# Performance work log

Measured on AMD Instinct MI355X. Metric: run time of the kernel, lower is better.

## Reference

```python
import jax, jax.numpy as jnp
import numpy as np

WIN = 9
EPS = 1e-05


def _box_sum(x, win=WIN):
    # Separable 3D box-filter sum: mathematically identical to conv3d with a
    pad = win // 2
    for axis in range(3):  # spatial axes D, H, W
        kshape = [1, 1, 1]
        kshape[axis] = win
        filt = jnp.ones((1, 1, *kshape), dtype=x.dtype)  # OIDHW
        padding = [(pad, pad) if i == axis else (0, 0) for i in range(3)]
        x = jax.lax.conv_general_dilated(
            x, filt, window_strides=(1, 1, 1), padding=padding,
            dimension_numbers=('NCDHW', 'OIDHW', 'NCDHW'))
    return x


def setup_inputs() -> dict:
    key = jax.random.key(0)
    k1, k2 = jax.random.split(key)
    shape = (2, 1, 160, 192, 224)
    y_true = jax.random.uniform(k1, shape, dtype=jnp.float32)
    y_pred = jax.random.uniform(k2, shape, dtype=jnp.float32)
    return {"y_true": y_true, "y_pred": y_pred}


def reference(y_true, y_pred):
    ii, ji = y_true, y_pred
    win_size = jnp.asarray(float(WIN ** 3), dtype=ii.dtype)

    i_sum = _box_sum(ii)
    j_sum = _box_sum(ji)
    i2_sum = _box_sum(ii * ii)
    j2_sum = _box_sum(ji * ji)
    ij_sum = _box_sum(ii * ji)

    ui = i_sum / win_size
    uj = j_sum / win_size
    cross = ij_sum - uj * i_sum - ui * j_sum + ui * uj * win_size
    i_var = jnp.maximum(i2_sum - 2 * ui * i_sum + ui * ui * win_size, EPS)
    j_var = jnp.maximum(j2_sum - 2 * uj * j_sum + uj * uj * win_size, EPS)
    return -jnp.mean(cross * cross / (i_var * j_var))
```

## Files before the change

kernel.cpp:

```cpp
#include <hip/hip_runtime.h>

namespace {

constexpr int BD = 2;
constexpr int DD = 160, HH = 192, WW = 224;
constexpr float INV_WIN = 1.0f / 729.0f;
constexpr float EPSV = 1e-5f;

constexpr int TH = 16, TW = 16;
constexpr int DC = 16;
constexpr int NREAL = DC + 8;
constexpr int NPAIR = NREAL / 2;
constexpr int NCH = DD / DC;
constexpr int GX = WW / TW;
constexpr int GY = HH / TH;
constexpr int GZ = BD * NCH;
constexpr int NBLK = GX * GY * GZ;
constexpr int NXCD = 8;
constexpr int CPX = NBLK / NXCD;
constexpr double NTOT = (double)BD * DD * HH * WW;

constexpr int SR_FS = 452;
constexpr int SR_PL = 2280;
constexpr int SC_FS = 324;
constexpr int SC_PL = 1620;

}

__global__ __launch_bounds__(256)
void ncc_fused(const float* __restrict__ x, const float* __restrict__ y,
               float* __restrict__ bsum) {
  const int tid = threadIdx.x;

  const int lid = (int)blockIdx.x;
  const int nl  = (lid & (NXCD - 1)) * CPX + (lid >> 3);
  const int zb  = nl / (GX * GY);
  const int rem = nl - zb * (GX * GY);
  const int by  = rem / GX;
  const int bx  = rem - by * GX;

  const int w0 = bx * TW;
  const int h0 = by * TH;
  const int b  = zb / NCH;
  const int d0 = (zb - b * NCH) * DC;

  __shared__ __align__(16) float srowF[2 * SR_PL];
  __shared__ __align__(16) float scolF[2 * SC_PL];
  __shared__ float swsum[4];

  const bool s2a = tid < 192;
  const int p2  = tid / 96;
  const int t96 = tid - 96 * p2;
  const int r2  = t96 >> 2;
  const int seg = tid & 3;
  const int gh  = h0 - 4 + r2;
  const int gw0 = w0 - 4 + seg * 4;
  const bool hok = (unsigned)gh < (unsigned)HH;
  const bool fastw = (gw0 >= 0) && (gw0 + 11 < WW);
  const unsigned plane = (unsigned)HH * WW;

  auto prefetch = [&](int s, float4* vx, float4* vy) {
    const int din = d0 - 4 + s;
    const float4 z = make_float4(0.f, 0.f, 0.f, 0.f);
    vx[0] = vx[1] = vx[2] = z;
    vy[0] = vy[1] = vy[2] = z;
    if (s2a && hok && (s < NREAL) && (din >= 0) && (din < DD)) {
      const unsigned rb = ((unsigned)b * DD + (unsigned)din) * plane + (unsigned)gh * WW;
      if (fastw) {
        const float4* px = (const float4*)(x + rb + gw0);
        const float4* py = (const float4*)(y + rb + gw0);
        vx[0] = px[0]; vx[1] = px[1]; vx[2] = px[2];
        vy[0] = py[0]; vy[1] = py[1]; vy[2] = py[2];
      } else {
        float* fx = (float*)vx;
        float* fy = (float*)vy;
#pragma unroll
        for (int e = 0; e < 12; ++e) {
          const int gw = gw0 + e;
          if ((unsigned)gw < (unsigned)WW) {
            fx[e] = x[rb + gw];
            fy[e] = y[rb + gw];
          }
        }
      }
    }
  };

  const int t3  = tid - 96;
  const int p3  = t3 / 80;
  const int r3  = t3 - 80 * p3;
  const int f3  = r3 >> 4;
  const int wl3 = r3 & 15;

  const int ow = tid & 15;
  const int oh = tid >> 4;

  float rg0[9], rg1[9], rg2[9], rg3[9], rg4[9];
#pragma unroll
  for (int k = 0; k < 9; ++k) { rg0[k]=0.f; rg1[k]=0.f; rg2[k]=0.f; rg3[k]=0.f; rg4[k]=0.f; }
  float a0=0.f, a1=0.f, a2=0.f, a3=0.f, a4=0.f;
  float lsum = 0.0f;

  float4 px4[3], py4[3];
  prefetch(p2, px4, py4);

#pragma unroll
  for (int ss = 0; ss <= NPAIR; ++ss) {
    float4 nx4[3], ny4[3];
    if (ss + 1 < NPAIR) prefetch(2 * (ss + 1) + p2, nx4, ny4);

    if (ss >= 1 && tid >= 96) {
      const float* rp = &srowF[p3 * SR_PL + f3 * SR_FS + wl3 * 28];
      float rv[24];
#pragma unroll
      for (int t = 0; t < 6; ++t) *(float4*)&rv[4 * t] = *(const float4*)&rp[4 * t];
      float acc = rv[0];
#pragma unroll
      for (int t = 1; t < 9; ++t) acc += rv[t];
      float ov[16];
      ov[0] = acc;
#pragma unroll
      for (int o = 1; o < 16; ++o) { acc += rv[o + 8] - rv[o - 1]; ov[o] = acc; }
      float* cp = &scolF[p3 * SC_PL + f3 * SC_FS + wl3 * 20];
#pragma unroll
      for (int t = 0; t < 4; ++t)
        *(float4*)&cp[4 * t] = make_float4(ov[4*t], ov[4*t+1], ov[4*t+2], ov[4*t+3]);
    }
    __syncthreads();

    if (ss < NPAIR && s2a) {
      float xv[12], yv[12];
#pragma unroll
      for (int k = 0; k < 3; ++k) {
        *(float4*)&xv[4 * k] = px4[k];
        *(float4*)&yv[4 * k] = py4[k];
      }
      float s0=0.f, s1=0.f, s2=0.f, s3=0.f, s4=0.f;
#pragma unroll
      for (int k = 0; k < 9; ++k) {
        s0 += xv[k]; s1 += yv[k];
        s2 = fmaf(xv[k], xv[k], s2);
        s3 = fmaf(yv[k], yv[k], s3);
        s4 = fmaf(xv[k], yv[k], s4);
      }
      float* wb = &srowF[p2 * SR_PL + (seg * 4) * 28 + r2];
      wb[0 * SR_FS] = s0; wb[1 * SR_FS] = s1; wb[2 * SR_FS] = s2;
      wb[3 * SR_FS] = s3; wb[4 * SR_FS] = s4;
#pragma unroll
      for (int t = 1; t < 4; ++t) {
        const float xn = xv[8 + t], xo = xv[t - 1];
        const float yn = yv[8 + t], yo = yv[t - 1];
        s0 += xn - xo;
        s1 += yn - yo;
        s2 += fmaf(xn, xn, -(xo * xo));
        s3 += fmaf(yn, yn, -(yo * yo));
        s4 += fmaf(xn, yn, -(xo * yo));
        float* wt = wb + t * 28;
        wt[0 * SR_FS] = s0; wt[1 * SR_FS] = s1; wt[2 * SR_FS] = s2;
        wt[3 * SR_FS] = s3; wt[4 * SR_FS] = s4;
      }
    }

    if (ss >= 1) {
      const int sA  = 2 * (ss - 1);
      const int sB  = sA + 1;
      const int slA = sA % 9;
      const int slB = sB % 9;
      const float* cA = &scolF[ow * 20 + oh];
      const float* cB = cA + SC_PL;
      const float gA0 = cA[0*SC_FS], gA1 = cA[1*SC_FS], gA2 = cA[2*SC_FS],
                  gA3 = cA[3*SC_FS], gA4 = cA[4*SC_FS];
      const float gB0 = cB[0*SC_FS], gB1 = cB[1*SC_FS], gB2 = cB[2*SC_FS],
                  gB3 = cB[3*SC_FS], gB4 = cB[4*SC_FS];

      a0 += gA0 - rg0[slA]; rg0[slA] = gA0;
      a1 += gA1 - rg1[slA]; rg1[slA] = gA1;
      a2 += gA2 - rg2[slA]; rg2[slA] = gA2;
      a3 += gA3 - rg3[slA]; rg3[slA] = gA3;
      a4 += gA4 - rg4[slA]; rg4[slA] = gA4;
      if (sA >= 8) {
        const float cross = fmaf(-a0 * INV_WIN, a1, a4);
        const float iv = fmaxf(fmaf(-a0 * INV_WIN, a0, a2), EPSV);
        const float jv = fmaxf(fmaf(-a1 * INV_WIN, a1, a3), EPSV);
        lsum += (cross * cross) / (iv * jv);
      }
      a0 += gB0 - rg0[slB]; rg0[slB] = gB0;
      a1 += gB1 - rg1[slB]; rg1[slB] = gB1;
      a2 += gB2 - rg2[slB]; rg2[slB] = gB2;
      a3 += gB3 - rg3[slB]; rg3[slB] = gB3;
      a4 += gB4 - rg4[slB]; rg4[slB] = gB4;
      if (sB >= 8) {
        const float cross = fmaf(-a0 * INV_WIN, a1, a4);
        const float iv = fmaxf(fmaf(-a0 * INV_WIN, a0, a2), EPSV);
        const float jv = fmaxf(fmaf(-a1 * INV_WIN, a1, a3), EPSV);
        lsum += (cross * cross) / (iv * jv);
      }
    }
    __syncthreads();
    if (ss + 1 < NPAIR) {
#pragma unroll
      for (int k = 0; k < 3; ++k) { px4[k] = nx4[k]; py4[k] = ny4[k]; }
    }
  }

#pragma unroll
  for (int off = 32; off > 0; off >>= 1) lsum += __shfl_down(lsum, off);
  if ((tid & 63) == 0) swsum[tid >> 6] = lsum;
  __syncthreads();
  if (tid == 0) bsum[nl] = swsum[0] + swsum[1] + swsum[2] + swsum[3];
}

__global__ __launch_bounds__(256)
void ncc_finalize(const float* __restrict__ bsum, float* __restrict__ out) {
  double s = 0.0;
  for (int i = threadIdx.x; i < NBLK; i += 256) s += (double)bsum[i];
#pragma unroll
  for (int off = 32; off > 0; off >>= 1) s += __shfl_down(s, off);
  __shared__ double sh[4];
  if ((threadIdx.x & 63) == 0) sh[threadIdx.x >> 6] = s;
  __syncthreads();
  if (threadIdx.x == 0)
    out[0] = (float)(-(sh[0] + sh[1] + sh[2] + sh[3]) / NTOT);
}

extern "C" void kernel_launch(void* const* d_in, const int* in_sizes, int n_in,
                              void* d_out, int out_size, void* d_ws, size_t ws_size,
                              hipStream_t stream) {
  const float* x = (const float*)d_in[0];
  const float* y = (const float*)d_in[1];
  float* bsum = (float*)d_ws;
  float* out  = (float*)d_out;

  ncc_fused<<<dim3(NBLK), dim3(256), 0, stream>>>(x, y, bsum);
  ncc_finalize<<<1, dim3(256), 0, stream>>>(bsum, out);
}
```

Baseline: 213.6 us.

## Double-buffer shared stages to pipeline row, column and depth passes with one barrier

Doubles the shared row and column buffers and skews the three stages across iterations so each loop step needs only one __syncthreads instead of two. The depth-accumulation stage now consumes column results produced in the previous step while new row sums are written to the alternate buffer. This removes a barrier per step and lets independent stages overlap, at the cost of doubling LDS usage, which may reduce blocks resident per CU, and adding one extra loop iteration.

```diff
diff --git a/kernel.cpp b/kernel.cpp
--- a/kernel.cpp
+++ b/kernel.cpp
@@ -44,8 +44,8 @@
   const int b  = zb / NCH;
   const int d0 = (zb - b * NCH) * DC;
 
-  __shared__ __align__(16) float srowF[2 * SR_PL];
-  __shared__ __align__(16) float scolF[2 * SC_PL];
+  __shared__ __align__(16) float srowF[2][2 * SR_PL];
+  __shared__ __align__(16) float scolF[2][2 * SC_PL];
   __shared__ float swsum[4];
 
   const bool s2a = tid < 192;
@@ -105,45 +105,37 @@
   prefetch(p2, px4, py4);
 
 #pragma unroll
-  for (int ss = 0; ss <= NPAIR; ++ss) {
+  for (int k = 0; k <= NPAIR + 1; ++k) {
     float4 nx4[3], ny4[3];
-    if (ss + 1 < NPAIR) prefetch(2 * (ss + 1) + p2, nx4, ny4);
-
-    if (ss >= 1 && tid >= 96) {
-      const float* rp = &srowF[p3 * SR_PL + f3 * SR_FS + wl3 * 28];
-      float rv[24];
-#pragma unroll
-      for (int t = 0; t < 6; ++t) *(float4*)&rv[4 * t] = *(const float4*)&rp[4 * t];
-      float acc = rv[0];
-#pragma unroll
-      for (int t = 1; t < 9; ++t) acc += rv[t];
-      float ov[16];
-      ov[0] = acc;
-#pragma unroll
-      for (int o = 1; o < 16; ++o) { acc += rv[o + 8] - rv[o - 1]; ov[o] = acc; }
-      float* cp = &scolF[p3 * SC_PL + f3 * SC_FS + wl3 * 20];
-#pragma unroll
-      for (int t = 0; t < 4; ++t)
-        *(float4*)&cp[4 * t] = make_float4(ov[4*t], ov[4*t+1], ov[4*t+2], ov[4*t+3]);
-    }
-    __syncthreads();
-
-    if (ss < NPAIR && s2a) {
+    if (k + 1 < NPAIR) prefetch(2 * (k + 1) + p2, nx4, ny4);
+
+    float gA0=0.f, gA1=0.f, gA2=0.f, gA3=0.f, gA4=0.f;
+    float gB0=0.f, gB1=0.f, gB2=0.f, gB3=0.f, gB4=0.f;
+    if (k >= 2) {
+      const float* cA = &scolF[k & 1][ow * 20 + oh];
+      const float* cB = cA + SC_PL;
+      gA0 = cA[0*SC_FS]; gA1 = cA[1*SC_FS]; gA2 = cA[2*SC_FS];
+      gA3 = cA[3*SC_FS]; gA4 = cA[4*SC_FS];
+      gB0 = cB[0*SC_FS]; gB1 = cB[1*SC_FS]; gB2 = cB[2*SC_FS];
+      gB3 = cB[3*SC_FS]; gB4 = cB[4*SC_FS];
+    }
+
+    if (k < NPAIR && s2a) {
       float xv[12], yv[12];
 #pragma unroll
-      for (int k = 0; k < 3; ++k) {
-        *(float4*)&xv[4 * k] = px4[k];
-        *(float4*)&yv[4 * k] = py4[k];
+      for (int q = 0; q < 3; ++q) {
+        *(float4*)&xv[4 * q] = px4[q];
+        *(float4*)&yv[4 * q] = py4[q];
       }
       float s0=0.f, s1=0.f, s2=0.f, s3=0.f, s4=0.f;
 #pragma unroll
-      for (int k = 0; k < 9; ++k) {
-        s0 += xv[k]; s1 += yv[k];
-        s2 = fmaf(xv[k], xv[k], s2);
-        s3 = fmaf(yv[k], yv[k], s3);
-        s4 = fmaf(xv[k], yv[k], s4);
-      }
-      float* wb = &srowF[p2 * SR_PL + (seg * 4) * 28 + r2];
+      for (int q = 0; q < 9; ++q) {
+        s0 += xv[q]; s1 += yv[q];
+        s2 = fmaf(xv[q], xv[q], s2);
+        s3 = fmaf(yv[q], yv[q], s3);
+        s4 = fmaf(xv[q], yv[q], s4);
+      }
+      float* wb = &srowF[k & 1][p2 * SR_PL + (seg * 4) * 28 + r2];
       wb[0 * SR_FS] = s0; wb[1 * SR_FS] = s1; wb[2 * SR_FS] = s2;
       wb[3 * SR_FS] = s3; wb[4 * SR_FS] = s4;
 #pragma unroll
@@ -161,17 +153,29 @@
       }
     }
 
-    if (ss >= 1) {
-      const int sA  = 2 * (ss - 1);
+    if (k >= 1 && k <= NPAIR && tid >= 96) {
+      const float* rp = &srowF[(k - 1) & 1][p3 * SR_PL + f3 * SR_FS + wl3 * 28];
+      float rv[24];
+#pragma unroll
+      for (int t = 0; t < 6; ++t) *(float4*)&rv[4 * t] = *(const float4*)&rp[4 * t];
+      float acc = rv[0];
+#pragma unroll
+      for (int t = 1; t < 9; ++t) acc += rv[t];
+      float ov[16];
+      ov[0] = acc;
+#pragma unroll
+      for (int o = 1; o < 16; ++o) { acc += rv[o + 8] - rv[o - 1]; ov[o] = acc; }
+      float* cp = &scolF[(k - 1) & 1][p3 * SC_PL + f3 * SC_FS + wl3 * 20];
+#pragma unroll
+      for (int t = 0; t < 4; ++t)
+        *(float4*)&cp[4 * t] = make_float4(ov[4*t], ov[4*t+1], ov[4*t+2], ov[4*t+3]);
+    }
+
+    if (k >= 2) {
+      const int sA  = 2 * (k - 2);
       const int sB  = sA + 1;
       const int slA = sA % 9;
       const int slB = sB % 9;
-      const float* cA = &scolF[ow * 20 + oh];
-      const float* cB = cA + SC_PL;
-      const float gA0 = cA[0*SC_FS], gA1 = cA[1*SC_FS], gA2 = cA[2*SC_FS],
-                  gA3 = cA[3*SC_FS], gA4 = cA[4*SC_FS];
-      const float gB0 = cB[0*SC_FS], gB1 = cB[1*SC_FS], gB2 = cB[2*SC_FS],
-                  gB3 = cB[3*SC_FS], gB4 = cB[4*SC_FS];
 
       a0 += gA0 - rg0[slA]; rg0[slA] = gA0;
       a1 += gA1 - rg1[slA]; rg1[slA] = gA1;
@@ -196,10 +200,11 @@
         lsum += (cross * cross) / (iv * jv);
       }
     }
+
     __syncthreads();
-    if (ss + 1 < NPAIR) {
-#pragma unroll
-      for (int k = 0; k < 3; ++k) { px4[k] = nx4[k]; py4[k] = ny4[k]; }
+    if (k + 1 < NPAIR) {
+#pragma unroll
+      for (int q = 0; q < 3; ++q) { px4[q] = nx4[q]; py4[q] = ny4[q]; }
     }
   }
 
```

Measured after the change: 212.1 us. Within noise of the previous version (-0.7%).
